# Kernel optimization log

Hardware: AMD Instinct MI355X
Metric: run time of the kernel (lower is better)

The kernel has to match this reference:

```python
import jax, jax.numpy as jnp
import numpy as np

N = 20000      # nodes
E = 640000     # edges (avg degree 32)
F = 128        # hidden_channels == num_filters
RBF = 64       # num_rbf
H = 8          # num_heads
DH = F // H    # head dim
T = 5          # number of distinct element types present in z
CUT = 5.0      # cutoff_upper (cutoff_lower = 0)


def setup_inputs() -> dict:
    key = jax.random.key(0)
    ks = jax.random.split(key, 20)
    s = 0.05
    inp = {
        "x": jax.random.normal(ks[0], (N, F), jnp.float32),
        "z": jax.random.randint(ks[1], (N,), 0, T, jnp.int32),
        "edge_index": jax.random.randint(ks[2], (2, E), 0, N, jnp.int32),
        "edge_weight": jax.random.uniform(ks[3], (E,), jnp.float32) * CUT,
        "edge_attr": jax.random.normal(ks[4], (E, RBF), jnp.float32),
        # ElemConv params
        "lin1_w": jax.random.normal(ks[5], (F, F), jnp.float32) / np.sqrt(F),
        "f_w1": jax.random.normal(ks[6], (F, RBF), jnp.float32) / np.sqrt(RBF),
        "f_b1": jnp.zeros((F,), jnp.float32),
        "f_w2": jax.random.normal(ks[7], (F, F), jnp.float32) / np.sqrt(F),
        "f_b2": jnp.zeros((F,), jnp.float32),
        # ElemAttn params
        "q_w": jax.random.normal(ks[8], (F, F), jnp.float32) / np.sqrt(F),
        "q_b": jax.random.normal(ks[9], (F,), jnp.float32) * s,
        "k_w": jax.random.normal(ks[10], (F, F), jnp.float32) / np.sqrt(F),
        "k_b": jax.random.normal(ks[11], (F,), jnp.float32) * s,
        "v_w": jax.random.normal(ks[12], (F, F), jnp.float32) / np.sqrt(F),
        "v_b": jax.random.normal(ks[13], (F,), jnp.float32) * s,
        "o1_w": jax.random.normal(ks[14], (F, F), jnp.float32) / np.sqrt(F),
        "o1_b": jax.random.normal(ks[15], (F,), jnp.float32) * s,
        "o2_w": jax.random.normal(ks[16], (F, F), jnp.float32) / np.sqrt(F),
        "o2_b": jax.random.normal(ks[17], (F,), jnp.float32) * s,
    }
    return inp


def reference(x, z, edge_index, edge_weight, edge_attr,
              lin1_w, f_w1, f_b1, f_w2, f_b2,
              q_w, q_b, k_w, k_b, v_w, v_b, o1_w, o1_b, o2_w, o2_b):
    silu = jax.nn.silu
    src, dst = edge_index[0], edge_index[1]

    # ---- ElemConv ----
    # CosineCutoff (cutoff_lower = 0)
    C = 0.5 * (jnp.cos(edge_weight * (jnp.pi / CUT)) + 1.0)
    C = C * (edge_weight < CUT).astype(x.dtype)
    # filter_net(edge_attr) * C
    W = silu(edge_attr @ f_w1.T + f_b1) @ f_w2.T + f_b2          # [E, F]
    W = W * C[:, None]
    xl = x @ lin1_w.T                                             # [N, F]
    msg = xl[src] * W                                             # [E, F]
    # aggregate by unique (z_j, dst) pair == dense [N, T] slot grid
    seg = dst * T + z[src]                                        # [E]
    y = jax.ops.segment_sum(msg, seg, num_segments=N * T).reshape(N, T, F)
    cnt = jax.ops.segment_sum(jnp.ones((E,), x.dtype), seg, num_segments=N * T)
    pm = (cnt > 0).astype(x.dtype).reshape(N, T)                  # presence mask

    # ---- ElemAttn (block-diagonal per target node over present slots) ----
    q = (y @ q_w.T + q_b).reshape(N, T, H, DH)
    k = (y @ k_w.T + k_b).reshape(N, T, H, DH)
    v = (y @ v_w.T + v_b).reshape(N, T, H, DH)
    attn = silu(jnp.einsum('nihd,njhd->nhij', q, k))              # [N, H, T, T]
    attn = attn * (pm[:, None, :, None] * pm[:, None, None, :])
    out = jnp.einsum('nhij,njhd->nihd', attn, v).reshape(N, T, F)
    out = out @ o1_w.T + o1_b                                     # [N, T, F]
    node = jnp.einsum('ntf,nt->nf', out, pm)                      # scatter-add by node
    return silu(node @ o2_w.T + o2_b)                             # [N, F]
```

## Files before the change

kernel.cpp:

```cpp
#include <hip/hip_runtime.h>

#define N_NODES 20000
#define E_EDGES 640000
#define F_DIM 128
#define RBF_DIM 64
#define T_TYPES 5
#define NSEG (N_NODES * T_TYPES)
#define EPB 128

typedef __attribute__((ext_vector_type(8))) short short8;
typedef __attribute__((ext_vector_type(4))) float f32x4;

__device__ __forceinline__ float silu_f(float x) { return x / (1.0f + __expf(-x)); }

__device__ __forceinline__ ushort f2bf(float f) {
  unsigned u = __float_as_uint(f);
  u += 0x7fffu + ((u >> 16) & 1u);
  return (ushort)(u >> 16);
}
__device__ __forceinline__ float bf2f(ushort u) {
  return __uint_as_float(((unsigned)u) << 16);
}
__device__ __forceinline__ unsigned cvt_pk(float lo, float hi) {
  unsigned r;
  asm("v_cvt_pk_bf16_f32 %0, %1, %2" : "=v"(r) : "v"(lo), "v"(hi));
  return r;
}
union S8U4 {
  short8 s;
  unsigned u[4];
};

__global__ __launch_bounds__(256) void prep_kernel(
    const float* __restrict__ w1, const float* __restrict__ w2,
    const float* __restrict__ qw, const float* __restrict__ kw,
    const float* __restrict__ vw, const float* __restrict__ o1w,
    const float* __restrict__ o2w, const float* __restrict__ lw,
    ushort* __restrict__ w1b, ushort* __restrict__ w2b,
    ushort* __restrict__ qwb, ushort* __restrict__ kwb,
    ushort* __restrict__ vwb, ushort* __restrict__ o1wb,
    ushort* __restrict__ o2wb, ushort* __restrict__ lwb) {
  int i = blockIdx.x * 256 + threadIdx.x;
  if (i < F_DIM * RBF_DIM) w1b[i] = f2bf(w1[i]);
  if (i < F_DIM * F_DIM) {
    w2b[i] = f2bf(w2[i]);
    qwb[i] = f2bf(qw[i]);
    kwb[i] = f2bf(kw[i]);
    vwb[i] = f2bf(vw[i]);
    o1wb[i] = f2bf(o1w[i]);
    o2wb[i] = f2bf(o2w[i]);
    lwb[i] = f2bf(lw[i]);
  }
}

__global__ __launch_bounds__(256) void hist_rank_kernel(
    const int* __restrict__ srcp, const int* __restrict__ dstp,
    const int* __restrict__ z, int* __restrict__ hist, int* __restrict__ rnk) {
  int e = blockIdx.x * 256 + threadIdx.x;
  int s = srcp[e];
  int seg = dstp[e] * T_TYPES + z[s];
  rnk[e] = atomicAdd(&hist[seg], 1);
}

__global__ __launch_bounds__(256) void scan1_kernel(const int* __restrict__ hist,
                                                    int* __restrict__ offs,
                                                    int* __restrict__ bsums) {
  __shared__ int lds[256];
  int tid = threadIdx.x;
  int base = blockIdx.x * 1024 + tid * 4;
  int v[4];
  int s = 0;
#pragma unroll
  for (int i = 0; i < 4; ++i) {
    v[i] = (base + i < NSEG) ? hist[base + i] : 0;
    s += v[i];
  }
  lds[tid] = s;
  __syncthreads();
  for (int d = 1; d < 256; d <<= 1) {
    int t = (tid >= d) ? lds[tid - d] : 0;
    __syncthreads();
    lds[tid] += t;
    __syncthreads();
  }
  int excl = lds[tid] - s;
#pragma unroll
  for (int i = 0; i < 4; ++i) {
    if (base + i < NSEG) offs[base + i] = excl;
    excl += v[i];
  }
  if (tid == 255) bsums[blockIdx.x] = lds[255];
}

__global__ __launch_bounds__(128) void scan2_kernel(int* __restrict__ bsums,
                                                    int nb) {
  __shared__ int lds[128];
  int tid = threadIdx.x;
  int v = (tid < nb) ? bsums[tid] : 0;
  lds[tid] = v;
  __syncthreads();
  for (int d = 1; d < 128; d <<= 1) {
    int t = (tid >= d) ? lds[tid - d] : 0;
    __syncthreads();
    lds[tid] += t;
    __syncthreads();
  }
  if (tid < nb) bsums[tid] = lds[tid] - v;
}

__global__ __launch_bounds__(256) void scatter_kernel(
    const int* __restrict__ srcp, const int* __restrict__ dstp,
    const int* __restrict__ z, const int* __restrict__ offs,
    const int* __restrict__ bsums, const int* __restrict__ rnk,
    int* __restrict__ perm) {
  int e = blockIdx.x * 256 + threadIdx.x;
  int s = srcp[e];
  int seg = dstp[e] * T_TYPES + z[s];
  perm[offs[seg] + bsums[seg >> 10] + rnk[e]] = e;
}

__global__ __launch_bounds__(256) void lin1_kernel(const float* __restrict__ x,
                                                   const ushort* __restrict__ lwb,
                                                   ushort* __restrict__ xlb) {
  const int tid = threadIdx.x;
  const int lane = tid & 63;
  const int w = tid >> 6;
  const int lr = lane & 15, lh = lane >> 4;
  const int r0 = blockIdx.x * 80;

  f32x4 acc[5][2] = {};
#pragma unroll
  for (int ksi = 0; ksi < 4; ++ksi) {
    short8 B[2];
#pragma unroll
    for (int fc = 0; fc < 2; ++fc)
      B[fc] = *(const short8*)(lwb + (size_t)(w * 32 + fc * 16 + lr) * 128 +
                               ksi * 32 + lh * 8);
#pragma unroll
    for (int fm = 0; fm < 5; ++fm) {
      const float* ap =
          x + (size_t)(r0 + fm * 16 + lr) * 128 + ksi * 32 + lh * 8;
      float4 a0 = *(const float4*)ap;
      float4 a1 = *(const float4*)(ap + 4);
      S8U4 t;
      t.u[0] = cvt_pk(a0.x, a0.y);
      t.u[1] = cvt_pk(a0.z, a0.w);
      t.u[2] = cvt_pk(a1.x, a1.y);
      t.u[3] = cvt_pk(a1.z, a1.w);
#pragma unroll
      for (int fc = 0; fc < 2; ++fc)
        acc[fm][fc] = __builtin_amdgcn_mfma_f32_16x16x32_bf16(
            t.s, B[fc], acc[fm][fc], 0, 0, 0);
    }
  }
#pragma unroll
  for (int fm = 0; fm < 5; ++fm)
#pragma unroll
    for (int fc = 0; fc < 2; ++fc)
#pragma unroll
      for (int rp = 0; rp < 4; rp += 2) {
        int rrow = fm * 16 + lh * 4 + rp;
        int col = w * 32 + fc * 16 + lr;
        unsigned u = cvt_pk(acc[fm][fc][rp], acc[fm][fc][rp + 1]);
        xlb[(size_t)(r0 + rrow) * 128 + col] = (ushort)u;
        xlb[(size_t)(r0 + rrow + 1) * 128 + col] = (ushort)(u >> 16);
      }
}

__global__ __launch_bounds__(256, 4) void edge_mfma_kernel(
    const float* __restrict__ edge_attr, const int* __restrict__ srcp,
    const int* __restrict__ dstp, const float* __restrict__ ewp,
    const int* __restrict__ z, const int* __restrict__ perm,
    const ushort* __restrict__ w1b, const float* __restrict__ b1,
    const ushort* __restrict__ w2b, const float* __restrict__ b2,
    const ushort* __restrict__ xlb, float* __restrict__ y) {
  __shared__ ushort hs[128 * 136];
  __shared__ float sC[EPB];
  __shared__ int srcoff[EPB];
  __shared__ int sseg[EPB];
  __shared__ unsigned long long smask[2];

  const int tid = threadIdx.x;
  const int e0 = blockIdx.x * EPB;
  const int lane = tid & 63;
  const int w = tid >> 6;
  const int wm = w >> 1, wn = w & 1;
  const int lr = lane & 15, lh = lane >> 4;

  int prow[4];
#pragma unroll
  for (int fm = 0; fm < 4; ++fm) prow[fm] = perm[e0 + wm * 64 + fm * 16 + lr];

  float rb1[4], rb2[4];
#pragma unroll
  for (int fc = 0; fc < 4; ++fc) {
    int n = wn * 64 + fc * 16 + lr;
    rb1[fc] = b1[n];
    rb2[fc] = b2[n];
  }

  if (tid < EPB) {
    int e = perm[e0 + tid];
    int s = srcp[e];
    srcoff[tid] = s * 128;
    sseg[tid] = dstp[e] * T_TYPES + z[s];
    float wd = ewp[e];
    float c = 0.5f * (__cosf(wd * 0.6283185307179586f) + 1.0f);
    sC[tid] = (wd < 5.0f) ? c : 0.0f;
  }

  f32x4 acc[4][4] = {};
#pragma unroll
  for (int ks = 0; ks < 2; ++ks) {
    const int k0 = ks * 32;
    short8 af[4], bfr[4];
#pragma unroll
    for (int fm = 0; fm < 4; ++fm) {
      const float* ap = edge_attr + (size_t)prow[fm] * 64 + k0 + lh * 8;
      float4 a0 = *(const float4*)ap;
      float4 a1 = *(const float4*)(ap + 4);
      S8U4 t;
      t.u[0] = cvt_pk(a0.x, a0.y);
      t.u[1] = cvt_pk(a0.z, a0.w);
      t.u[2] = cvt_pk(a1.x, a1.y);
      t.u[3] = cvt_pk(a1.z, a1.w);
      af[fm] = t.s;
    }
#pragma unroll
    for (int fc = 0; fc < 4; ++fc)
      bfr[fc] = *(const short8*)(w1b + (size_t)(wn * 64 + fc * 16 + lr) * 64 +
                                 k0 + lh * 8);
#pragma unroll
    for (int fm = 0; fm < 4; ++fm)
#pragma unroll
      for (int fc = 0; fc < 4; ++fc)
        acc[fm][fc] = __builtin_amdgcn_mfma_f32_16x16x32_bf16(
            af[fm], bfr[fc], acc[fm][fc], 0, 0, 0);
  }

#pragma unroll
  for (int fm = 0; fm < 4; ++fm) {
#pragma unroll
    for (int fc = 0; fc < 4; ++fc) {
#pragma unroll
      for (int rp = 0; rp < 4; rp += 2) {
        int ml0 = wm * 64 + fm * 16 + lh * 4 + rp;
        int ml1 = ml0 + 1;
        int n = wn * 64 + fc * 16 + lr;
        float h0 = silu_f(acc[fm][fc][rp] + rb1[fc]);
        float h1 = silu_f(acc[fm][fc][rp + 1] + rb1[fc]);
        unsigned u = cvt_pk(h0, h1);
        hs[(ml0 * 256 + ((n * 2) ^ ((ml0 & 7) << 4))) >> 1] = (ushort)u;
        hs[(ml1 * 256 + ((n * 2) ^ ((ml1 & 7) << 4))) >> 1] = (ushort)(u >> 16);
      }
    }
  }
  __syncthreads();

  if (tid < EPB) {
    int head = (tid == 0) || (sseg[tid] != sseg[tid - 1]);
    unsigned long long m = __ballot(head);
    if ((tid & 63) == 0) smask[tid >> 6] = m;
  }

  f32x4 acc2[4][4] = {};
#pragma unroll
  for (int ks = 0; ks < 4; ++ks) {
    const int k0 = ks * 32;
    short8 af[4], bfr[4];
#pragma unroll
    for (int fm = 0; fm < 4; ++fm) {
      int ml = wm * 64 + fm * 16 + lr;
      int byte_in_row = (k0 * 2 + lh * 16) ^ ((ml & 7) << 4);
      af[fm] = *(const short8*)&hs[(ml * 256 + byte_in_row) >> 1];
    }
#pragma unroll
    for (int fc = 0; fc < 4; ++fc)
      bfr[fc] = *(const short8*)(w2b + (size_t)(wn * 64 + fc * 16 + lr) * 128 +
                                 k0 + lh * 8);
#pragma unroll
    for (int fm = 0; fm < 4; ++fm)
#pragma unroll
      for (int fc = 0; fc < 4; ++fc)
        acc2[fm][fc] = __builtin_amdgcn_mfma_f32_16x16x32_bf16(
            af[fm], bfr[fc], acc2[fm][fc], 0, 0, 0);
  }
  __syncthreads();

#pragma unroll
  for (int fm = 0; fm < 4; ++fm) {
#pragma unroll
    for (int rp = 0; rp < 4; rp += 2) {
      int ml0 = wm * 64 + fm * 16 + lh * 4 + rp;
      float c0 = sC[ml0], c1 = sC[ml0 + 1];
#pragma unroll
      for (int fc = 0; fc < 4; ++fc) {
        int n = wn * 64 + fc * 16 + lr;
        float v0 = (acc2[fm][fc][rp] + rb2[fc]) * c0;
        float v1 = (acc2[fm][fc][rp + 1] + rb2[fc]) * c1;
        *(unsigned*)&hs[n * 136 + ml0] = cvt_pk(v0, v1);
      }
    }
  }
  __syncthreads();

  {
    int cp = tid & 63;
    int q = tid >> 6;
    int rbase = q * 32;
    int c0 = cp * 2;
    unsigned mm = (unsigned)(smask[q >> 1] >> ((q & 1) * 32));
    float a0 = 0.0f, a1 = 0.0f;
    int cur = sseg[rbase];
    bool first = true;
#pragma unroll
    for (int it = 0; it < 4; ++it) {
      int r0 = rbase + it * 8;
      short8 m0 = *(const short8*)&hs[c0 * 136 + r0];
      short8 m1 = *(const short8*)&hs[(c0 + 1) * 136 + r0];
      unsigned xv[8];
#pragma unroll
      for (int j = 0; j < 8; ++j)
        xv[j] = *(const unsigned*)&xlb[(size_t)srcoff[r0 + j] + c0];
#pragma unroll
      for (int j = 0; j < 8; ++j) {
        int rr = it * 8 + j;
        if (rr && ((mm >> rr) & 1u)) {
          float* yp = &y[(size_t)cur * 128 + c0];
          if (first) {
            atomicAdd(yp, a0);
            atomicAdd(yp + 1, a1);
            first = false;
          } else {
            yp[0] = a0;
            yp[1] = a1;
          }
          a0 = a1 = 0.0f;
          cur = sseg[r0 + j];
        }
        a0 += bf2f((ushort)m0[j]) * bf2f((ushort)xv[j]);
        a1 += bf2f((ushort)m1[j]) * bf2f((ushort)(xv[j] >> 16));
      }
    }
    float* yp = &y[(size_t)cur * 128 + c0];
    atomicAdd(yp, a0);
    atomicAdd(yp + 1, a1);
  }
}

#define QS 136
#define NB 16
__global__ __launch_bounds__(256) void attn_out_kernel(
    const float* __restrict__ y, const int* __restrict__ hist,
    const ushort* __restrict__ qwb, const ushort* __restrict__ kwb,
    const ushort* __restrict__ vwb, const float* __restrict__ qb,
    const float* __restrict__ kb, const float* __restrict__ vb,
    const ushort* __restrict__ o1wb, const float* __restrict__ o1b,
    const ushort* __restrict__ o2wb, const float* __restrict__ o2b,
    float* __restrict__ outp) {
  __shared__ ushort bufA[80 * QS];
  __shared__ ushort bufB[80 * QS];
  __shared__ float aap[NB * 8 * 2 * 5];
  __shared__ float pmv[80];
  __shared__ float snpm[NB];
  __shared__ float sxb[3][128];

  const int tid = threadIdx.x;
  const int xcd = blockIdx.x & 7;
  const int loc = blockIdx.x >> 3;
  const int bid = (xcd < 2 ? xcd * 157 : 314 + (xcd - 2) * 156) + loc;
  const int n0 = bid * NB;
  const int row0 = n0 * T_TYPES;
  const int lane = tid & 63;
  const int w = tid >> 6;
  const int lr = lane & 15, lh = lane >> 4;

  if (tid < 128) {
    sxb[0][tid] = qb[tid];
    sxb[1][tid] = kb[tid];
    sxb[2][tid] = vb[tid];
  }
  if (tid < 80) pmv[tid] = (hist[(size_t)row0 + tid] > 0) ? 1.0f : 0.0f;

  short8 A[4][5];
#pragma unroll
  for (int ksi = 0; ksi < 4; ++ksi) {
#pragma unroll
    for (int fm = 0; fm < 5; ++fm) {
      const float* ap =
          y + (size_t)(row0 + fm * 16 + lr) * 128 + ksi * 32 + lh * 8;
      float4 a0 = *(const float4*)ap;
      float4 a1 = *(const float4*)(ap + 4);
      S8U4 t;
      t.u[0] = cvt_pk(a0.x, a0.y);
      t.u[1] = cvt_pk(a0.z, a0.w);
      t.u[2] = cvt_pk(a1.x, a1.y);
      t.u[3] = cvt_pk(a1.z, a1.w);
      A[ksi][fm] = t.s;
    }
  }
  __syncthreads();
  if (tid < NB) {
    float s = 0.0f;
#pragma unroll
    for (int t = 0; t < 5; ++t) s += pmv[tid * 5 + t];
    snpm[tid] = s;
  }

  auto do_proj = [&](const ushort* __restrict__ Wb, const float* bias_row,
                     ushort* __restrict__ dst) {
    f32x4 acc[5][2] = {};
#pragma unroll
    for (int ksi = 0; ksi < 4; ++ksi) {
      short8 B[2];
#pragma unroll
      for (int fc = 0; fc < 2; ++fc)
        B[fc] = *(const short8*)(Wb + (size_t)(w * 32 + fc * 16 + lr) * 128 +
                                 ksi * 32 + lh * 8);
#pragma unroll
      for (int fm = 0; fm < 5; ++fm)
#pragma unroll
        for (int fc = 0; fc < 2; ++fc)
          acc[fm][fc] = __builtin_amdgcn_mfma_f32_16x16x32_bf16(
              A[ksi][fm], B[fc], acc[fm][fc], 0, 0, 0);
    }
#pragma unroll
    for (int fm = 0; fm < 5; ++fm)
#pragma unroll
      for (int fc = 0; fc < 2; ++fc)
#pragma unroll
        for (int rp = 0; rp < 4; rp += 2) {
          int rrow = fm * 16 + lh * 4 + rp;
          int col = w * 32 + fc * 16 + lr;
          float v0 = acc[fm][fc][rp] + bias_row[col];
          float v1 = acc[fm][fc][rp + 1] + bias_row[col];
          unsigned u = cvt_pk(v0, v1);
          dst[rrow * QS + col] = (ushort)u;
          dst[(rrow + 1) * QS + col] = (ushort)(u >> 16);
        }
  };

  do_proj(qwb, sxb[0], bufA);
  do_proj(kwb, sxb[1], bufB);
  __syncthreads();

  {
    int n = tid >> 4, h = (tid >> 1) & 7, g = tid & 1;
    int i0 = g ? 3 : 0;
    int cnt = g ? 2 : 3;
    float kv[5][16];
#pragma unroll
    for (int j = 0; j < 5; ++j) {
      short8 v0 = *(const short8*)&bufB[(n * 5 + j) * QS + h * 16];
      short8 v1 = *(const short8*)&bufB[(n * 5 + j) * QS + h * 16 + 8];
#pragma unroll
      for (int d = 0; d < 8; ++d) {
        kv[j][d] = bf2f((ushort)v0[d]);
        kv[j][d + 8] = bf2f((ushort)v1[d]);
      }
    }
    float a[5] = {};
    for (int ii = 0; ii < cnt; ++ii) {
      int i = i0 + ii;
      float qv[16];
      short8 q0 = *(const short8*)&bufA[(n * 5 + i) * QS + h * 16];
      short8 q1 = *(const short8*)&bufA[(n * 5 + i) * QS + h * 16 + 8];
#pragma unroll
      for (int d = 0; d < 8; ++d) {
        qv[d] = bf2f((ushort)q0[d]);
        qv[d + 8] = bf2f((ushort)q1[d]);
      }
      float pmi = pmv[n * 5 + i];
#pragma unroll
      for (int j = 0; j < 5; ++j) {
        float dd = 0.0f;
#pragma unroll
        for (int d = 0; d < 16; ++d) dd += qv[d] * kv[j][d];
        a[j] += pmi * silu_f(dd);
      }
    }
#pragma unroll
    for (int j = 0; j < 5; ++j) aap[((n * 8 + h) * 2 + g) * 5 + j] = a[j];
  }
  __syncthreads();

  do_proj(vwb, sxb[2], bufA);
  __syncthreads();

  {
    int n = tid >> 4;
    int o = tid & 15;
    int f0 = o * 8;
    int h = f0 >> 4;
    float acc8[8] = {};
#pragma unroll
    for (int j = 0; j < 5; ++j) {
      float a = (aap[((n * 8 + h) * 2 + 0) * 5 + j] +
                 aap[((n * 8 + h) * 2 + 1) * 5 + j]) *
                pmv[n * 5 + j];
      short8 vv8 = *(const short8*)&bufA[(n * 5 + j) * QS + f0];
#pragma unroll
      for (int d = 0; d < 8; ++d) acc8[d] += a * bf2f((ushort)vv8[d]);
    }
    S8U4 t;
    t.u[0] = cvt_pk(acc8[0], acc8[1]);
    t.u[1] = cvt_pk(acc8[2], acc8[3]);
    t.u[2] = cvt_pk(acc8[4], acc8[5]);
    t.u[3] = cvt_pk(acc8[6], acc8[7]);
    *(short8*)&bufB[n * QS + f0] = t.s;
  }
  __syncthreads();

  {
    f32x4 acc[2] = {};
#pragma unroll
    for (int ksi = 0; ksi < 4; ++ksi) {
      short8 af = *(const short8*)&bufB[lr * QS + ksi * 32 + lh * 8];
      short8 B0 = *(const short8*)(o1wb + (size_t)(w * 32 + lr) * 128 +
                                   ksi * 32 + lh * 8);
      short8 B1 = *(const short8*)(o1wb + (size_t)(w * 32 + 16 + lr) * 128 +
                                   ksi * 32 + lh * 8);
      acc[0] = __builtin_amdgcn_mfma_f32_16x16x32_bf16(af, B0, acc[0], 0, 0, 0);
      acc[1] = __builtin_amdgcn_mfma_f32_16x16x32_bf16(af, B1, acc[1], 0, 0, 0);
    }
#pragma unroll
    for (int fc = 0; fc < 2; ++fc) {
      int col = w * 32 + fc * 16 + lr;
      float bb = o1b[col];
#pragma unroll
      for (int r = 0; r < 4; ++r) {
        int row = lh * 4 + r;
        bufA[row * QS + col] = f2bf(acc[fc][r] + snpm[row] * bb);
      }
    }
  }
  __syncthreads();

  {
    f32x4 acc[2] = {};
#pragma unroll
    for (int ksi = 0; ksi < 4; ++ksi) {
      short8 af = *(const short8*)&bufA[lr * QS + ksi * 32 + lh * 8];
      short8 B0 = *(const short8*)(o2wb + (size_t)(w * 32 + lr) * 128 +
                                   ksi * 32 + lh * 8);
      short8 B1 = *(const short8*)(o2wb + (size_t)(w * 32 + 16 + lr) * 128 +
                                   ksi * 32 + lh * 8);
      acc[0] = __builtin_amdgcn_mfma_f32_16x16x32_bf16(af, B0, acc[0], 0, 0, 0);
      acc[1] = __builtin_amdgcn_mfma_f32_16x16x32_bf16(af, B1, acc[1], 0, 0, 0);
    }
#pragma unroll
    for (int fc = 0; fc < 2; ++fc) {
      int col = w * 32 + fc * 16 + lr;
      float bb = o2b[col];
#pragma unroll
      for (int r = 0; r < 4; ++r) {
        int row = lh * 4 + r;
        outp[(size_t)(n0 + row) * 128 + col] = silu_f(acc[fc][r] + bb);
      }
    }
  }
}

extern "C" void kernel_launch(void* const* d_in, const int* in_sizes, int n_in,
                              void* d_out, int out_size, void* d_ws, size_t ws_size,
                              hipStream_t stream) {
  const float* x = (const float*)d_in[0];
  const int* z = (const int*)d_in[1];
  const int* ei = (const int*)d_in[2];
  const float* ew = (const float*)d_in[3];
  const float* ea = (const float*)d_in[4];
  const float* lin1_w = (const float*)d_in[5];
  const float* fw1 = (const float*)d_in[6];
  const float* fb1 = (const float*)d_in[7];
  const float* fw2 = (const float*)d_in[8];
  const float* fb2 = (const float*)d_in[9];
  const float* qw = (const float*)d_in[10];
  const float* qb = (const float*)d_in[11];
  const float* kw = (const float*)d_in[12];
  const float* kb = (const float*)d_in[13];
  const float* vw = (const float*)d_in[14];
  const float* vb = (const float*)d_in[15];
  const float* o1w = (const float*)d_in[16];
  const float* o1b = (const float*)d_in[17];
  const float* o2w = (const float*)d_in[18];
  const float* o2b = (const float*)d_in[19];
  float* outp = (float*)d_out;
  float* ws = (float*)d_ws;

  float* y = ws;
  ushort* xlb = (ushort*)(y + (size_t)NSEG * F_DIM);
  ushort* w1b = xlb + (size_t)N_NODES * F_DIM;
  ushort* w2b = w1b + F_DIM * RBF_DIM;
  ushort* qwb = w2b + F_DIM * F_DIM;
  ushort* kwb = qwb + F_DIM * F_DIM;
  ushort* vwb = kwb + F_DIM * F_DIM;
  ushort* o1wb = vwb + F_DIM * F_DIM;
  ushort* o2wb = o1wb + F_DIM * F_DIM;
  ushort* lwb = o2wb + F_DIM * F_DIM;
  int* hist = (int*)(lwb + F_DIM * F_DIM);
  int* offs = hist + NSEG;
  int* bsums = offs + NSEG;
  int* rnk = bsums + 128;
  int* perm = rnk + E_EDGES;

  const int* srcp = ei;
  const int* dstp = ei + E_EDGES;
  const int NB_SCAN = (NSEG + 1023) / 1024;

  hipMemsetAsync(y, 0, (size_t)NSEG * F_DIM * sizeof(float), stream);
  hipMemsetAsync(hist, 0, (size_t)NSEG * sizeof(int), stream);

  prep_kernel<<<64, 256, 0, stream>>>(fw1, fw2, qw, kw, vw, o1w, o2w, lin1_w,
                                      w1b, w2b, qwb, kwb, vwb, o1wb, o2wb, lwb);
  hist_rank_kernel<<<E_EDGES / 256, 256, 0, stream>>>(srcp, dstp, z, hist, rnk);
  scan1_kernel<<<NB_SCAN, 256, 0, stream>>>(hist, offs, bsums);
  scan2_kernel<<<1, 128, 0, stream>>>(bsums, NB_SCAN);
  scatter_kernel<<<E_EDGES / 256, 256, 0, stream>>>(srcp, dstp, z, offs, bsums,
                                                    rnk, perm);
  lin1_kernel<<<N_NODES / 80, 256, 0, stream>>>(x, lwb, xlb);
  edge_mfma_kernel<<<E_EDGES / EPB, 256, 0, stream>>>(ea, srcp, dstp, ew, z, perm,
                                                      w1b, fb1, w2b, fb2, xlb, y);
  attn_out_kernel<<<N_NODES / NB, 256, 0, stream>>>(y, hist, qwb, kwb, vwb, qb, kb,
                                                    vb, o1wb, o1b, o2wb, o2b, outp);
}
```

Measured before the change: 303.5 us.

## Fuse memsets and lin1 into stage kernels, presort edge metadata in scatter

Drops the two hipMemsetAsync calls: the hist buffer is zeroed inside prep_kernel and the y buffer is zeroed by the histogram blocks of a new fused stage1 kernel. lin1 now runs as extra blocks of that same launch. scatter_kernel also writes the segment id, source offset and cosine cutoff in sorted order, so edge_mfma reads them contiguously instead of gathering through perm. This cuts launch count and random gathers, at the cost of extra workspace and writes in scatter.

```diff
diff --git a/kernel.cpp b/kernel.cpp
--- a/kernel.cpp
+++ b/kernel.cpp
@@ -39,7 +39,8 @@
     ushort* __restrict__ w1b, ushort* __restrict__ w2b,
     ushort* __restrict__ qwb, ushort* __restrict__ kwb,
     ushort* __restrict__ vwb, ushort* __restrict__ o1wb,
-    ushort* __restrict__ o2wb, ushort* __restrict__ lwb) {
+    ushort* __restrict__ o2wb, ushort* __restrict__ lwb,
+    int* __restrict__ hist) {
   int i = blockIdx.x * 256 + threadIdx.x;
   if (i < F_DIM * RBF_DIM) w1b[i] = f2bf(w1[i]);
   if (i < F_DIM * F_DIM) {
@@ -51,15 +52,69 @@
     o2wb[i] = f2bf(o2w[i]);
     lwb[i] = f2bf(lw[i]);
   }
-}
-
-__global__ __launch_bounds__(256) void hist_rank_kernel(
+  for (int j = i; j < NSEG; j += 64 * 256) hist[j] = 0;
+}
+
+__global__ __launch_bounds__(256) void stage1_kernel(
     const int* __restrict__ srcp, const int* __restrict__ dstp,
-    const int* __restrict__ z, int* __restrict__ hist, int* __restrict__ rnk) {
-  int e = blockIdx.x * 256 + threadIdx.x;
-  int s = srcp[e];
-  int seg = dstp[e] * T_TYPES + z[s];
-  rnk[e] = atomicAdd(&hist[seg], 1);
+    const int* __restrict__ z, int* __restrict__ hist, int* __restrict__ rnk,
+    float* __restrict__ y, const float* __restrict__ x,
+    const ushort* __restrict__ lwb, ushort* __restrict__ xlb) {
+  const int b = blockIdx.x;
+  const int tid = threadIdx.x;
+  if (b < E_EDGES / 256) {
+    int e = b * 256 + tid;
+    int s = srcp[e];
+    int seg = dstp[e] * T_TYPES + z[s];
+    rnk[e] = atomicAdd(&hist[seg], 1);
+    float4* yz = (float4*)(y + (size_t)b * 5120);
+#pragma unroll
+    for (int i = 0; i < 5; ++i)
+      yz[tid + i * 256] = make_float4(0.f, 0.f, 0.f, 0.f);
+  } else {
+    const int lane = tid & 63;
+    const int w = tid >> 6;
+    const int lr = lane & 15, lh = lane >> 4;
+    const int r0 = (b - E_EDGES / 256) * 80;
+
+    f32x4 acc[5][2] = {};
+#pragma unroll
+    for (int ksi = 0; ksi < 4; ++ksi) {
+      short8 B[2];
+#pragma unroll
+      for (int fc = 0; fc < 2; ++fc)
+        B[fc] = *(const short8*)(lwb + (size_t)(w * 32 + fc * 16 + lr) * 128 +
+                                 ksi * 32 + lh * 8);
+#pragma unroll
+      for (int fm = 0; fm < 5; ++fm) {
+        const float* ap =
+            x + (size_t)(r0 + fm * 16 + lr) * 128 + ksi * 32 + lh * 8;
+        float4 a0 = *(const float4*)ap;
+        float4 a1 = *(const float4*)(ap + 4);
+        S8U4 t;
+        t.u[0] = cvt_pk(a0.x, a0.y);
+        t.u[1] = cvt_pk(a0.z, a0.w);
+        t.u[2] = cvt_pk(a1.x, a1.y);
+        t.u[3] = cvt_pk(a1.z, a1.w);
+#pragma unroll
+        for (int fc = 0; fc < 2; ++fc)
+          acc[fm][fc] = __builtin_amdgcn_mfma_f32_16x16x32_bf16(
+              t.s, B[fc], acc[fm][fc], 0, 0, 0);
+      }
+    }
+#pragma unroll
+    for (int fm = 0; fm < 5; ++fm)
+#pragma unroll
+      for (int fc = 0; fc < 2; ++fc)
+#pragma unroll
+        for (int rp = 0; rp < 4; rp += 2) {
+          int rrow = fm * 16 + lh * 4 + rp;
+          int col = w * 32 + fc * 16 + lr;
+          unsigned u = cvt_pk(acc[fm][fc][rp], acc[fm][fc][rp + 1]);
+          xlb[(size_t)(r0 + rrow) * 128 + col] = (ushort)u;
+          xlb[(size_t)(r0 + rrow + 1) * 128 + col] = (ushort)(u >> 16);
+        }
+  }
 }
 
 __global__ __launch_bounds__(256) void scan1_kernel(const int* __restrict__ hist,
@@ -110,70 +165,30 @@
 
 __global__ __launch_bounds__(256) void scatter_kernel(
     const int* __restrict__ srcp, const int* __restrict__ dstp,
-    const int* __restrict__ z, const int* __restrict__ offs,
-    const int* __restrict__ bsums, const int* __restrict__ rnk,
-    int* __restrict__ perm) {
+    const int* __restrict__ z, const float* __restrict__ ewp,
+    const int* __restrict__ offs, const int* __restrict__ bsums,
+    const int* __restrict__ rnk, int* __restrict__ perm,
+    int* __restrict__ ssegS, int* __restrict__ srcS,
+    float* __restrict__ sCS) {
   int e = blockIdx.x * 256 + threadIdx.x;
   int s = srcp[e];
   int seg = dstp[e] * T_TYPES + z[s];
-  perm[offs[seg] + bsums[seg >> 10] + rnk[e]] = e;
-}
-
-__global__ __launch_bounds__(256) void lin1_kernel(const float* __restrict__ x,
-                                                   const ushort* __restrict__ lwb,
-                                                   ushort* __restrict__ xlb) {
-  const int tid = threadIdx.x;
-  const int lane = tid & 63;
-  const int w = tid >> 6;
-  const int lr = lane & 15, lh = lane >> 4;
-  const int r0 = blockIdx.x * 80;
-
-  f32x4 acc[5][2] = {};
-#pragma unroll
-  for (int ksi = 0; ksi < 4; ++ksi) {
-    short8 B[2];
-#pragma unroll
-    for (int fc = 0; fc < 2; ++fc)
-      B[fc] = *(const short8*)(lwb + (size_t)(w * 32 + fc * 16 + lr) * 128 +
-                               ksi * 32 + lh * 8);
-#pragma unroll
-    for (int fm = 0; fm < 5; ++fm) {
-      const float* ap =
-          x + (size_t)(r0 + fm * 16 + lr) * 128 + ksi * 32 + lh * 8;
-      float4 a0 = *(const float4*)ap;
-      float4 a1 = *(const float4*)(ap + 4);
-      S8U4 t;
-      t.u[0] = cvt_pk(a0.x, a0.y);
-      t.u[1] = cvt_pk(a0.z, a0.w);
-      t.u[2] = cvt_pk(a1.x, a1.y);
-      t.u[3] = cvt_pk(a1.z, a1.w);
-#pragma unroll
-      for (int fc = 0; fc < 2; ++fc)
-        acc[fm][fc] = __builtin_amdgcn_mfma_f32_16x16x32_bf16(
-            t.s, B[fc], acc[fm][fc], 0, 0, 0);
-    }
-  }
-#pragma unroll
-  for (int fm = 0; fm < 5; ++fm)
-#pragma unroll
-    for (int fc = 0; fc < 2; ++fc)
-#pragma unroll
-      for (int rp = 0; rp < 4; rp += 2) {
-        int rrow = fm * 16 + lh * 4 + rp;
-        int col = w * 32 + fc * 16 + lr;
-        unsigned u = cvt_pk(acc[fm][fc][rp], acc[fm][fc][rp + 1]);
-        xlb[(size_t)(r0 + rrow) * 128 + col] = (ushort)u;
-        xlb[(size_t)(r0 + rrow + 1) * 128 + col] = (ushort)(u >> 16);
-      }
+  int pos = offs[seg] + bsums[seg >> 10] + rnk[e];
+  perm[pos] = e;
+  ssegS[pos] = seg;
+  srcS[pos] = s * 128;
+  float wd = ewp[e];
+  float c = 0.5f * (__cosf(wd * 0.6283185307179586f) + 1.0f);
+  sCS[pos] = (wd < 5.0f) ? c : 0.0f;
 }
 
 __global__ __launch_bounds__(256, 4) void edge_mfma_kernel(
-    const float* __restrict__ edge_attr, const int* __restrict__ srcp,
-    const int* __restrict__ dstp, const float* __restrict__ ewp,
-    const int* __restrict__ z, const int* __restrict__ perm,
-    const ushort* __restrict__ w1b, const float* __restrict__ b1,
-    const ushort* __restrict__ w2b, const float* __restrict__ b2,
-    const ushort* __restrict__ xlb, float* __restrict__ y) {
+    const float* __restrict__ edge_attr, const int* __restrict__ perm,
+    const int* __restrict__ ssegS, const int* __restrict__ srcS,
+    const float* __restrict__ sCS, const ushort* __restrict__ w1b,
+    const float* __restrict__ b1, const ushort* __restrict__ w2b,
+    const float* __restrict__ b2, const ushort* __restrict__ xlb,
+    float* __restrict__ y) {
   __shared__ ushort hs[128 * 136];
   __shared__ float sC[EPB];
   __shared__ int srcoff[EPB];
@@ -200,13 +215,10 @@
   }
 
   if (tid < EPB) {
-    int e = perm[e0 + tid];
-    int s = srcp[e];
-    srcoff[tid] = s * 128;
-    sseg[tid] = dstp[e] * T_TYPES + z[s];
-    float wd = ewp[e];
-    float c = 0.5f * (__cosf(wd * 0.6283185307179586f) + 1.0f);
-    sC[tid] = (wd < 5.0f) ? c : 0.0f;
+    int p = e0 + tid;
+    srcoff[tid] = srcS[p];
+    sseg[tid] = ssegS[p];
+    sC[tid] = sCS[p];
   }
 
   f32x4 acc[4][4] = {};
@@ -602,24 +614,26 @@
   int* bsums = offs + NSEG;
   int* rnk = bsums + 128;
   int* perm = rnk + E_EDGES;
+  int* ssegS = perm + E_EDGES;
+  int* srcS = ssegS + E_EDGES;
+  float* sCS = (float*)(srcS + E_EDGES);
 
   const int* srcp = ei;
   const int* dstp = ei + E_EDGES;
   const int NB_SCAN = (NSEG + 1023) / 1024;
 
-  hipMemsetAsync(y, 0, (size_t)NSEG * F_DIM * sizeof(float), stream);
-  hipMemsetAsync(hist, 0, (size_t)NSEG * sizeof(int), stream);
-
   prep_kernel<<<64, 256, 0, stream>>>(fw1, fw2, qw, kw, vw, o1w, o2w, lin1_w,
-                                      w1b, w2b, qwb, kwb, vwb, o1wb, o2wb, lwb);
-  hist_rank_kernel<<<E_EDGES / 256, 256, 0, stream>>>(srcp, dstp, z, hist, rnk);
+                                      w1b, w2b, qwb, kwb, vwb, o1wb, o2wb, lwb,
+                                      hist);
+  stage1_kernel<<<E_EDGES / 256 + N_NODES / 80, 256, 0, stream>>>(
+      srcp, dstp, z, hist, rnk, y, x, lwb, xlb);
   scan1_kernel<<<NB_SCAN, 256, 0, stream>>>(hist, offs, bsums);
   scan2_kernel<<<1, 128, 0, stream>>>(bsums, NB_SCAN);
-  scatter_kernel<<<E_EDGES / 256, 256, 0, stream>>>(srcp, dstp, z, offs, bsums,
-                                                    rnk, perm);
-  lin1_kernel<<<N_NODES / 80, 256, 0, stream>>>(x, lwb, xlb);
-  edge_mfma_kernel<<<E_EDGES / EPB, 256, 0, stream>>>(ea, srcp, dstp, ew, z, perm,
-                                                      w1b, fb1, w2b, fb2, xlb, y);
-  attn_out_kernel<<<N_NODES / NB, 256, 0, stream>>>(y, hist, qwb, kwb, vwb, qb, kb,
-                                                    vb, o1wb, o1b, o2wb, o2b, outp);
-}
+  scatter_kernel<<<E_EDGES / 256, 256, 0, stream>>>(
+      srcp, dstp, z, ew, offs, bsums, rnk, perm, ssegS, srcS, sCS);
+  edge_mfma_kernel<<<E_EDGES / EPB, 256, 0, stream>>>(
+      ea, perm, ssegS, srcS, sCS, w1b, fb1, w2b, fb2, xlb, y);
+  attn_out_kernel<<<N_NODES / NB, 256, 0, stream>>>(y, hist, qwb, kwb, vwb, qb,
+                                                    kb, vb, o1wb, o1b, o2wb,
+                                                    o2b, outp);
+}
```

Result: faster. 292.2 us (-3.7%).
